# Kernel optimization log

Hardware: AMD Instinct MI355X
Metric: run time of the kernel (lower is better)

Reference implementation:

```python
import jax, jax.numpy as jnp
import numpy as np

N_NODES = 100000
N_EDGES = 1600000


def _graphconv(h, src, dst, norm_src, norm_dst, W, b, n_nodes):
    # DGL GraphConv, norm='both': D_dst^{-1/2} * A * (D_src^{-1/2} * h) @ W + b, then relu
    h = h * norm_src[:, None]
    agg = jax.ops.segment_sum(h[src], dst, num_segments=n_nodes)  # [N, d] SpMM
    rst = agg @ W  # in_feats <= out_feats path: aggregate first, then W
    rst = rst * norm_dst[:, None]
    rst = rst + b
    return jax.nn.relu(rst)


def setup_inputs() -> dict:
    key = jax.random.key(0)
    ks = jax.random.split(key, 12)
    H = 64
    features = jax.random.normal(ks[0], (N_NODES, H), dtype=jnp.float32)
    src = jax.random.randint(ks[1], (N_EDGES,), 0, N_NODES, dtype=jnp.int64 if jax.config.jax_enable_x64 else jnp.int32)
    dst = jax.random.randint(ks[2], (N_EDGES,), 0, N_NODES, dtype=jnp.int64 if jax.config.jax_enable_x64 else jnp.int32)
    sc = 1.0 / np.sqrt(H)
    W1 = jax.random.normal(ks[3], (H, H), dtype=jnp.float32) * sc
    b1 = jnp.zeros((H,), dtype=jnp.float32)
    W2 = jax.random.normal(ks[4], (H, H), dtype=jnp.float32) * sc
    b2 = jnp.zeros((H,), dtype=jnp.float32)
    W3 = jax.random.normal(ks[5], (H, H), dtype=jnp.float32) * sc
    b3 = jnp.zeros((H,), dtype=jnp.float32)
    Wc = jax.random.normal(ks[6], (H, 10), dtype=jnp.float32) * sc
    bc = jnp.zeros((10,), dtype=jnp.float32)
    return {"features": features, "src": src, "dst": dst,
            "W1": W1, "b1": b1, "W2": W2, "b2": b2, "W3": W3, "b3": b3,
            "Wc": Wc, "bc": bc}


def reference(features, src, dst, W1, b1, W2, b2, W3, b3, Wc, bc):
    n = features.shape[0]
    ones = jnp.ones_like(src, dtype=features.dtype)
    deg_out = jax.ops.segment_sum(ones, src, num_segments=n)
    deg_in = jax.ops.segment_sum(ones, dst, num_segments=n)
    norm_src = jnp.clip(deg_out, 1.0) ** -0.5  # allow_zero_in_degree: clamp(min=1)
    norm_dst = jnp.clip(deg_in, 1.0) ** -0.5
    h = features
    for W, b in ((W1, b1), (W2, b2), (W3, b3)):
        # dropout p=0.0 / eval mode -> identity
        h = _graphconv(h, src, dst, norm_src, norm_dst, W, b, n)
    hg = jnp.mean(h, axis=0, keepdims=True)  # AvgPooling over the single graph -> [1, H]
    logits = hg @ Wc + bc  # [1, n_classes]
    return (logits, hg)
```

## Files before the change

### kernel.cpp

```cpp
#include <hip/hip_runtime.h>
#include <hip/hip_fp8.h>


__global__ void build_kernel(const int* __restrict__ src, const int* __restrict__ dst,
                             int* __restrict__ deg_out, int* __restrict__ cursor,
                             int* __restrict__ csr_src, int E) {
  int i = blockIdx.x * blockDim.x + threadIdx.x;
  if (i < E) {
    int s = src[i];
    int d = dst[i];
    atomicAdd(&deg_out[s], 1);
    int p = atomicAdd(&cursor[d], 1);
    if (p < 64) csr_src[(size_t)d * 64 + p] = s;
  }
}

__global__ void pad_kernel(const int* __restrict__ cnt, int* __restrict__ csr_src, int N) {
  int i = blockIdx.x * blockDim.x + threadIdx.x;
  int n = i >> 6;
  int slot = i & 63;
  if (n < N) {
    int deg = min(cnt[n], 64);
    int pend = min((deg + 7) & ~7, 64);
    if (slot >= deg && slot < pend) csr_src[(size_t)n * 64 + slot] = N;
  }
}

__device__ __forceinline__ unsigned char f32_to_fp8(float f) {
  __hip_fp8_e4m3 q(f);
  return (unsigned char)q.__x;
}

__device__ __forceinline__ float fp8_to_f32(unsigned char v) {
  __hip_fp8_e4m3 q;
  q.__x = (__hip_fp8_storage_t)v;
  return (float)q;
}

__device__ __forceinline__ float rl_f(float v, int srclane) {
  return __uint_as_float(__builtin_amdgcn_readlane(__float_as_uint(v), srclane));
}

__global__ __launch_bounds__(256) void gemm_scale_kernel(
    const float* __restrict__ h, const float* __restrict__ W,
    const int* __restrict__ deg_out, unsigned char* __restrict__ g, int N) {
  int lane = threadIdx.x & 63;
  int wave = (blockIdx.x << 2) + (threadIdx.x >> 6);
  int nwaves = gridDim.x << 2;
  float wcol[64];
#pragma unroll
  for (int k = 0; k < 64; k++) wcol[k] = W[k * 64 + lane];
  for (int n = wave; n < N; n += nwaves) {
    int nu = __builtin_amdgcn_readfirstlane(n);
    float hval = h[(size_t)nu * 64 + lane];
    float acc = 0.f;
#pragma unroll
    for (int k = 0; k < 64; k++) acc = fmaf(rl_f(hval, k), wcol[k], acc);
    float val = acc * rsqrtf((float)max(deg_out[nu], 1));
    g[(size_t)nu * 64 + lane] = f32_to_fp8(val);
  }
}

#define GATHER16_RL(base)                                                      \
  {                                                                            \
    int s0 = __builtin_amdgcn_readlane(idxv, e + 0);                           \
    int s1 = __builtin_amdgcn_readlane(idxv, e + 1);                           \
    int s2 = __builtin_amdgcn_readlane(idxv, e + 2);                           \
    int s3 = __builtin_amdgcn_readlane(idxv, e + 3);                           \
    int s4 = __builtin_amdgcn_readlane(idxv, e + 4);                           \
    int s5 = __builtin_amdgcn_readlane(idxv, e + 5);                           \
    int s6 = __builtin_amdgcn_readlane(idxv, e + 6);                           \
    int s7 = __builtin_amdgcn_readlane(idxv, e + 7);                           \
    int s8 = __builtin_amdgcn_readlane(idxv, e + 8);                           \
    int s9 = __builtin_amdgcn_readlane(idxv, e + 9);                           \
    int sa = __builtin_amdgcn_readlane(idxv, e + 10);                          \
    int sb = __builtin_amdgcn_readlane(idxv, e + 11);                          \
    int sc = __builtin_amdgcn_readlane(idxv, e + 12);                          \
    int sd = __builtin_amdgcn_readlane(idxv, e + 13);                          \
    int se = __builtin_amdgcn_readlane(idxv, e + 14);                          \
    int sf = __builtin_amdgcn_readlane(idxv, e + 15);                          \
    unsigned char v0 = base[(size_t)s0 * 64 + lane];                           \
    unsigned char v1 = base[(size_t)s1 * 64 + lane];                           \
    unsigned char v2 = base[(size_t)s2 * 64 + lane];                           \
    unsigned char v3 = base[(size_t)s3 * 64 + lane];                           \
    unsigned char v4 = base[(size_t)s4 * 64 + lane];                           \
    unsigned char v5 = base[(size_t)s5 * 64 + lane];                           \
    unsigned char v6 = base[(size_t)s6 * 64 + lane];                           \
    unsigned char v7 = base[(size_t)s7 * 64 + lane];                           \
    unsigned char v8 = base[(size_t)s8 * 64 + lane];                           \
    unsigned char v9 = base[(size_t)s9 * 64 + lane];                           \
    unsigned char va = base[(size_t)sa * 64 + lane];                           \
    unsigned char vb = base[(size_t)sb * 64 + lane];                           \
    unsigned char vc = base[(size_t)sc * 64 + lane];                           \
    unsigned char vd = base[(size_t)sd * 64 + lane];                           \
    unsigned char ve = base[(size_t)se * 64 + lane];                           \
    unsigned char vf = base[(size_t)sf * 64 + lane];                           \
    acc += (((fp8_to_f32(v0) + fp8_to_f32(v1)) + (fp8_to_f32(v2) + fp8_to_f32(v3))) +   \
            ((fp8_to_f32(v4) + fp8_to_f32(v5)) + (fp8_to_f32(v6) + fp8_to_f32(v7)))) +  \
           (((fp8_to_f32(v8) + fp8_to_f32(v9)) + (fp8_to_f32(va) + fp8_to_f32(vb))) +   \
            ((fp8_to_f32(vc) + fp8_to_f32(vd)) + (fp8_to_f32(ve) + fp8_to_f32(vf))));   \
  }

#define GATHER8_RL(base)                                                       \
  {                                                                            \
    int s0 = __builtin_amdgcn_readlane(idxv, e + 0);                           \
    int s1 = __builtin_amdgcn_readlane(idxv, e + 1);                           \
    int s2 = __builtin_amdgcn_readlane(idxv, e + 2);                           \
    int s3 = __builtin_amdgcn_readlane(idxv, e + 3);                           \
    int s4 = __builtin_amdgcn_readlane(idxv, e + 4);                           \
    int s5 = __builtin_amdgcn_readlane(idxv, e + 5);                           \
    int s6 = __builtin_amdgcn_readlane(idxv, e + 6);                           \
    int s7 = __builtin_amdgcn_readlane(idxv, e + 7);                           \
    unsigned char v0 = base[(size_t)s0 * 64 + lane];                           \
    unsigned char v1 = base[(size_t)s1 * 64 + lane];                           \
    unsigned char v2 = base[(size_t)s2 * 64 + lane];                           \
    unsigned char v3 = base[(size_t)s3 * 64 + lane];                           \
    unsigned char v4 = base[(size_t)s4 * 64 + lane];                           \
    unsigned char v5 = base[(size_t)s5 * 64 + lane];                           \
    unsigned char v6 = base[(size_t)s6 * 64 + lane];                           \
    unsigned char v7 = base[(size_t)s7 * 64 + lane];                           \
    acc += ((fp8_to_f32(v0) + fp8_to_f32(v1)) + (fp8_to_f32(v2) + fp8_to_f32(v3))) +    \
           ((fp8_to_f32(v4) + fp8_to_f32(v5)) + (fp8_to_f32(v6) + fp8_to_f32(v7)));     \
  }

__global__ __launch_bounds__(256) void spmm_kernel(
    const unsigned char* __restrict__ g, const int* __restrict__ cnt,
    const int* __restrict__ csr_src, const float* __restrict__ bias,
    float* __restrict__ h_out, int N) {
  int lane = threadIdx.x & 63;
  int wave = (blockIdx.x << 2) + (threadIdx.x >> 6);
  int nwaves = gridDim.x << 2;
  float b = bias[lane];
  for (int w1 = wave; w1 < N; w1 += nwaves) {
    int w = __builtin_amdgcn_readfirstlane(w1);
    int deg = min(cnt[w], 64);
    int idxv = csr_src[(size_t)w * 64 + lane];
    int end = min((deg + 7) & ~7, 64);
    float acc = 0.f;
    int e = 0;
    for (; e + 16 <= end; e += 16) GATHER16_RL(g)
    if (e < end) GATHER8_RL(g)
    float r = acc * rsqrtf((float)max(deg, 1)) + b;
    h_out[(size_t)w * 64 + lane] = fmaxf(r, 0.f);
  }
}

__global__ __launch_bounds__(256) void spmm_pool_kernel(
    const unsigned char* __restrict__ g, const int* __restrict__ cnt,
    const int* __restrict__ csr_src, const float* __restrict__ bias,
    float* __restrict__ pool, int N) {
  int lane = threadIdx.x & 63;
  int wid = threadIdx.x >> 6;
  int wave = (blockIdx.x << 2) + wid;
  int nwaves = gridDim.x << 2;
  float b = bias[lane];
  float psum = 0.f;
  for (int w1 = wave; w1 < N; w1 += nwaves) {
    int w = __builtin_amdgcn_readfirstlane(w1);
    int deg = min(cnt[w], 64);
    int idxv = csr_src[(size_t)w * 64 + lane];
    int end = min((deg + 7) & ~7, 64);
    float acc = 0.f;
    int e = 0;
    for (; e + 16 <= end; e += 16) GATHER16_RL(g)
    if (e < end) GATHER8_RL(g)
    psum += fmaxf(acc * rsqrtf((float)max(deg, 1)) + b, 0.f);
  }
  __shared__ float red[4][64];
  red[wid][lane] = psum;
  __syncthreads();
  if (wid == 0) {
    float v = red[0][lane] + red[1][lane] + red[2][lane] + red[3][lane];
    atomicAdd(&pool[lane], v);
  }
}

__global__ void final_kernel(const float* __restrict__ pool, const float* __restrict__ Wc,
                             const float* __restrict__ bc, float* __restrict__ out, float invN) {
  int t = threadIdx.x;
  __shared__ float hg[64];
  float m = pool[t] * invN;
  hg[t] = m;
  out[10 + t] = m;
  __syncthreads();
  if (t < 10) {
    float s = bc[t];
#pragma unroll
    for (int k = 0; k < 64; k++) s = fmaf(hg[k], Wc[k * 10 + t], s);
    out[t] = s;
  }
}

extern "C" void kernel_launch(void* const* d_in, const int* in_sizes, int n_in,
                              void* d_out, int out_size, void* d_ws, size_t ws_size,
                              hipStream_t stream) {
  const float* features = (const float*)d_in[0];
  const int* src = (const int*)d_in[1];
  const int* dst = (const int*)d_in[2];
  const float* W1 = (const float*)d_in[3];
  const float* b1 = (const float*)d_in[4];
  const float* W2 = (const float*)d_in[5];
  const float* b2 = (const float*)d_in[6];
  const float* W3 = (const float*)d_in[7];
  const float* b3 = (const float*)d_in[8];
  const float* Wc = (const float*)d_in[9];
  const float* bc = (const float*)d_in[10];
  float* out = (float*)d_out;

  const int N = in_sizes[0] / 64;
  const int E = in_sizes[1];

  char* ws = (char*)d_ws;
  size_t off = 0;
  auto alloc = [&](size_t bytes) {
    void* p = ws + off;
    off = (off + bytes + 255) & ~(size_t)255;
    return p;
  };
  int* deg_out = (int*)alloc((size_t)N * 4);
  int* cursor = (int*)alloc((size_t)N * 4);
  float* pool = (float*)alloc(64 * 4);
  size_t zero_bytes = off;
  int* csr_src = (int*)alloc((size_t)N * 64 * 4);
  unsigned char* bufG = (unsigned char*)alloc((size_t)(N + 1) * 64);
  float* bufH = (float*)alloc((size_t)N * 64 * 4);

  hipMemsetAsync(d_ws, 0, zero_bytes, stream);
  hipMemsetAsync(bufG + (size_t)N * 64, 0, 64, stream);

  int eb = (E + 255) / 256;
  build_kernel<<<eb, 256, 0, stream>>>(src, dst, deg_out, cursor, csr_src, E);
  pad_kernel<<<(N * 64 + 255) / 256, 256, 0, stream>>>(cursor, csr_src, N);

  gemm_scale_kernel<<<2048, 256, 0, stream>>>(features, W1, deg_out, bufG, N);
  spmm_kernel<<<2048, 256, 0, stream>>>(bufG, cursor, csr_src, b1, bufH, N);
  gemm_scale_kernel<<<2048, 256, 0, stream>>>(bufH, W2, deg_out, bufG, N);
  spmm_kernel<<<2048, 256, 0, stream>>>(bufG, cursor, csr_src, b2, bufH, N);
  gemm_scale_kernel<<<2048, 256, 0, stream>>>(bufH, W3, deg_out, bufG, N);
  spmm_pool_kernel<<<2048, 256, 0, stream>>>(bufG, cursor, csr_src, b3, pool, N);
  final_kernel<<<1, 64, 0, stream>>>(pool, Wc, bc, out, 1.0f / (float)N);
}
```

Measured before the change: 472.5 us.

## Partition CSR build by node range and drop the pad kernel

The build kernel now uses 2048 blocks in 8 groups. Each group owns a node range and scans its share of edges, so the atomics and CSR writes for a given node range come from one set of blocks. This is meant to improve L2 locality of the atomic traffic, possibly splitting it across XCDs. The separate pad kernel is removed: the SpMM kernels now replace indices in lanes beyond the degree with the zero row N, which saves a kernel launch and a pass over the CSR. In exchange, every edge is read 8 times, once per node-range group.

```diff
diff --git a/kernel.cpp b/kernel.cpp
--- a/kernel.cpp
+++ b/kernel.cpp
@@ -2,27 +2,25 @@
 #include <hip/hip_fp8.h>
 
 
-__global__ void build_kernel(const int* __restrict__ src, const int* __restrict__ dst,
-                             int* __restrict__ deg_out, int* __restrict__ cursor,
-                             int* __restrict__ csr_src, int E) {
-  int i = blockIdx.x * blockDim.x + threadIdx.x;
-  if (i < E) {
+__global__ __launch_bounds__(256) void build_kernel(
+    const int* __restrict__ src, const int* __restrict__ dst,
+    int* __restrict__ deg_out, int* __restrict__ cursor,
+    int* __restrict__ csr_src, int E, int N) {
+  int r = blockIdx.x & 7;
+  int g = blockIdx.x >> 3;
+  int ngroups = gridDim.x >> 3;
+  int RS = (N + 7) >> 3;
+  int lo_n = r * RS, hi_n = min(lo_n + RS, N);
+  int per = (E + ngroups - 1) / ngroups;
+  int lo_e = g * per, hi_e = min(lo_e + per, E);
+  for (int i = lo_e + threadIdx.x; i < hi_e; i += 256) {
     int s = src[i];
     int d = dst[i];
-    atomicAdd(&deg_out[s], 1);
-    int p = atomicAdd(&cursor[d], 1);
-    if (p < 64) csr_src[(size_t)d * 64 + p] = s;
-  }
-}
-
-__global__ void pad_kernel(const int* __restrict__ cnt, int* __restrict__ csr_src, int N) {
-  int i = blockIdx.x * blockDim.x + threadIdx.x;
-  int n = i >> 6;
-  int slot = i & 63;
-  if (n < N) {
-    int deg = min(cnt[n], 64);
-    int pend = min((deg + 7) & ~7, 64);
-    if (slot >= deg && slot < pend) csr_src[(size_t)n * 64 + slot] = N;
+    if (s >= lo_n && s < hi_n) atomicAdd(&deg_out[s], 1);
+    if (d >= lo_n && d < hi_n) {
+      int p = atomicAdd(&cursor[d], 1);
+      if (p < 64) csr_src[(size_t)d * 64 + p] = s;
+    }
   }
 }
 
@@ -134,7 +132,8 @@
   for (int w1 = wave; w1 < N; w1 += nwaves) {
     int w = __builtin_amdgcn_readfirstlane(w1);
     int deg = min(cnt[w], 64);
-    int idxv = csr_src[(size_t)w * 64 + lane];
+    int rawv = csr_src[(size_t)w * 64 + lane];
+    int idxv = (lane < deg) ? rawv : N;
     int end = min((deg + 7) & ~7, 64);
     float acc = 0.f;
     int e = 0;
@@ -158,7 +157,8 @@
   for (int w1 = wave; w1 < N; w1 += nwaves) {
     int w = __builtin_amdgcn_readfirstlane(w1);
     int deg = min(cnt[w], 64);
-    int idxv = csr_src[(size_t)w * 64 + lane];
+    int rawv = csr_src[(size_t)w * 64 + lane];
+    int idxv = (lane < deg) ? rawv : N;
     int end = min((deg + 7) & ~7, 64);
     float acc = 0.f;
     int e = 0;
@@ -228,9 +228,7 @@
   hipMemsetAsync(d_ws, 0, zero_bytes, stream);
   hipMemsetAsync(bufG + (size_t)N * 64, 0, 64, stream);
 
-  int eb = (E + 255) / 256;
-  build_kernel<<<eb, 256, 0, stream>>>(src, dst, deg_out, cursor, csr_src, E);
-  pad_kernel<<<(N * 64 + 255) / 256, 256, 0, stream>>>(cursor, csr_src, N);
+  build_kernel<<<2048, 256, 0, stream>>>(src, dst, deg_out, cursor, csr_src, E, N);
 
   gemm_scale_kernel<<<2048, 256, 0, stream>>>(features, W1, deg_out, bufG, N);
   spmm_kernel<<<2048, 256, 0, stream>>>(bufG, cursor, csr_src, b1, bufH, N);
```

New measurement: 448.3 us. 1.05x faster.
